# Performance work log

Hardware: AMD Instinct MI355X
Metric: run time of the kernel (lower is better)

The kernel has to match this reference:

```python
import jax, jax.numpy as jnp
import numpy as np

B, D, H, O = 4096, 1024, 8192, 1000

def setup_inputs() -> dict:
    key = jax.random.key(0)
    k1, k2, k3 = jax.random.split(key, 3)
    x = jax.random.normal(k1, (B, D), dtype=jnp.float32)
    kohonen_weights = jax.random.normal(k2, (H, D), dtype=jnp.float32) * (6.0 / (H + D)) ** 0.5
    grossberg_weights = jax.random.normal(k3, (O, H), dtype=jnp.float32) * (6.0 / (O + H)) ** 0.5
    return {"x": x, "kohonen_weights": kohonen_weights, "grossberg_weights": grossberg_weights}

def reference(x, kohonen_weights, grossberg_weights):
    # but kept faithful since distances only feed argmin -> same winners either way)
    x_sq = jnp.sum(x * x, axis=1, keepdims=True)                      # [B,1]
    w_sq = jnp.sum(kohonen_weights * kohonen_weights, axis=1)         # [H]
    sq_dists = x_sq - 2.0 * (x @ kohonen_weights.T) + w_sq[None, :]   # [B,H]
    winners = jnp.argmin(sq_dists, axis=1)                            # [B]
    # one_hot @ grossberg.T is mathematically a row gather of grossberg.T
    output = grossberg_weights.T[winners]                             # [B,O]
    return output, winners
```

## Files before the change

### kernel.cpp

```cpp
#include <hip/hip_runtime.h>
#include <hip/hip_bf16.h>

#define B_ 4096
#define D_ 1024
#define H_ 8192
#define O_ 1000
#define K2 2048
#define NT 96

typedef __attribute__((ext_vector_type(8))) short short8;
typedef __attribute__((ext_vector_type(4))) short short4v;
typedef __attribute__((ext_vector_type(16))) float f32x16;

union BF4 { __hip_bfloat16 b[4]; short4v s; };

__device__ __forceinline__ void gload16(void* ldsp, const void* g) {
  __builtin_amdgcn_global_load_lds(
      (const __attribute__((address_space(1))) unsigned int*)g,
      (__attribute__((address_space(3))) unsigned int*)ldsp, 16, 0, 0);
}

__device__ __forceinline__ int aoff32_(int T) {
  const int g = T >> 1, t = g / 3, r = g - 3 * t;
  return (r == 1 ? 1024 : 0) + t * 64 + (T & 1) * 32;
}
__device__ __forceinline__ int boff32_(int T) {
  const int g = T >> 1, t = g / 3, r = g - 3 * t;
  return (r == 2 ? 1024 : 0) + t * 64 + (T & 1) * 32;
}

__global__ __launch_bounds__(256) void split_all_kernel(
    const float* __restrict__ x, const float* __restrict__ w,
    __hip_bfloat16* __restrict__ Ap, __hip_bfloat16* __restrict__ Bp,
    float* __restrict__ xsq, float* __restrict__ wsq,
    unsigned long long* __restrict__ keys)
{
  const int r = blockIdx.x;
  const int t = threadIdx.x;
  const float* src;
  __hip_bfloat16* dst;
  float* sq;
  if (r < B_) {
    src = x + (size_t)r * D_; dst = Ap + (size_t)r * K2; sq = xsq + r;
    if (t == 0) keys[r] = ~0ULL;
  } else {
    const int rr = r - B_;
    src = w + (size_t)rr * D_; dst = Bp + (size_t)rr * K2; sq = wsq + rr;
  }
  const float4 v = ((const float4*)src)[t];
  float ss = v.x * v.x + v.y * v.y + v.z * v.z + v.w * v.w;

  BF4 Hh, Ll;
  const float e[4] = {v.x, v.y, v.z, v.w};
#pragma unroll
  for (int i = 0; i < 4; ++i) {
    __hip_bfloat16 h = __float2bfloat16(e[i]);
    Hh.b[i] = h;
    Ll.b[i] = __float2bfloat16(e[i] - __bfloat162float(h));
  }
  *(short4v*)(dst + t * 4) = Hh.s;
  *(short4v*)(dst + 1024 + t * 4) = Ll.s;

#pragma unroll
  for (int o = 32; o > 0; o >>= 1) ss += __shfl_down(ss, o);
  __shared__ float wsum[4];
  if ((t & 63) == 0) wsum[t >> 6] = ss;
  __syncthreads();
  if (t == 0) *sq = (wsum[0] + wsum[1]) + (wsum[2] + wsum[3]);
}


#define BAR() do { asm volatile("" ::: "memory"); \
                   __builtin_amdgcn_s_barrier(); \
                   asm volatile("" ::: "memory"); } while (0)
#define SB0() __builtin_amdgcn_sched_barrier(0)
#define GATE_S(S) asm volatile("s_waitcnt vmcnt(" S ")" ::: "memory")
#define LGKM6() do { asm volatile("s_waitcnt lgkmcnt(6)"); SB0(); } while (0)
#define LGKM0() do { asm volatile("s_waitcnt lgkmcnt(0)"); SB0(); } while (0)

#define DSR(dst, base, OFF) \
  asm volatile("ds_read_b128 %0, %1 offset:" OFF : "=v"(dst) : "v"(base))

#define RDP(F, DSEL, KK) do { \
    const unsigned a_ = aB + (DSEL) + ofk##KK; \
    const unsigned b_ = bB + (DSEL) + ofk##KK; \
    DSR(F[0], a_, "0");    DSR(F[1], a_, "2048"); \
    DSR(F[2], a_, "4096"); DSR(F[3], a_, "6144"); \
    DSR(F[4], b_, "0");    DSR(F[5], b_, "2048"); \
  } while (0)

#define STAGE_A(T) do { \
    const int ka_ = aoff32_(T); \
    char* d_ = lds + ((T)&3)*32768 + wid*2048 + lane*16; \
    gload16(d_,        gA0 + ka_); \
    gload16(d_ + 1024, gA1 + ka_); } while (0)
#define STAGE_B(T) do { \
    const int kb_ = boff32_(T); \
    char* d_ = lds + ((T)&3)*32768 + 16384 + wid*2048 + lane*16; \
    gload16(d_,        gB0 + kb_); \
    gload16(d_ + 1024, gB1 + kb_); } while (0)

#define MFMA32(a, b, c) __builtin_amdgcn_mfma_f32_32x32x16_bf16(a, b, c, 0, 0, 0)

#define MMQ32(F) do { \
    __builtin_amdgcn_s_setprio(1); \
    acc[0][0] = MFMA32(F[0], F[4], acc[0][0]); \
    acc[0][1] = MFMA32(F[0], F[5], acc[0][1]); \
    acc[1][0] = MFMA32(F[1], F[4], acc[1][0]); \
    acc[1][1] = MFMA32(F[1], F[5], acc[1][1]); \
    acc[2][0] = MFMA32(F[2], F[4], acc[2][0]); \
    acc[2][1] = MFMA32(F[2], F[5], acc[2][1]); \
    acc[3][0] = MFMA32(F[3], F[4], acc[3][0]); \
    acc[3][1] = MFMA32(F[3], F[5], acc[3][1]); \
    __builtin_amdgcn_s_setprio(0); \
    SB0(); } while (0)

#define TILE(DSEL, D1SEL, T, DOSTAGE, GS, DONEXT) do { \
     \
    RDP(f1, DSEL, 1); \
    if (DOSTAGE) STAGE_A((T) + 3); \
    LGKM6(); \
    MMQ32(f0); \
     \
    if (DONEXT) RDP(f0, D1SEL, 0); \
    if (DOSTAGE) STAGE_B((T) + 3); \
    if (DONEXT) { LGKM6(); } else { LGKM0(); } \
    MMQ32(f1); \
    GATE_S(GS); BAR(); \
  } while (0)

__global__ __launch_bounds__(512, 2) void gemm_argmin_kernel(
    const __hip_bfloat16* __restrict__ Ap, const __hip_bfloat16* __restrict__ Bp,
    const float* __restrict__ xsq, const float* __restrict__ wsq,
    unsigned long long* __restrict__ keys)
{
  __shared__ char lds[131072];

  const int t = threadIdx.x;
  const int id = blockIdx.x;
  const int xcd = id & 7;
  const int r_ = id >> 3;
  const int by = (xcd >> 2) * 8 + (r_ >> 3);
  const int bx = (xcd & 3) * 8 + (r_ & 7);
  const int brow = by * 256, bcol = bx * 256;

  const int lane = t & 63, wid = t >> 6;
  const int wm = wid >> 2, wn = wid & 3;
  const int c31 = lane & 31;
  const int kh = lane >> 5;
  const unsigned fsw = (unsigned)((c31 >> 3) & 3);

  const unsigned ofk0 = (((0u + kh) ^ fsw) * 16);
  const unsigned ofk1 = (((2u + kh) ^ fsw) * 16);

  const unsigned lb = (unsigned)(uintptr_t)lds;
  const unsigned aB = lb + (unsigned)(wm * 8192 + c31 * 64);
  const unsigned bB = lb + (unsigned)(16384 + wn * 4096 + c31 * 64);

  const int sr = lane >> 2;
  const int su0 = (lane & 3) ^ (lane >> 5);
  const int su1 = su0 ^ 2;
  const __hip_bfloat16* gA0 = Ap + (size_t)(brow + wid * 32 + sr) * K2 + su0 * 8;
  const __hip_bfloat16* gA1 = Ap + (size_t)(brow + wid * 32 + 16 + sr) * K2 + su1 * 8;
  const __hip_bfloat16* gB0 = Bp + (size_t)(bcol + wid * 32 + sr) * K2 + su0 * 8;
  const __hip_bfloat16* gB1 = Bp + (size_t)(bcol + wid * 32 + 16 + sr) * K2 + su1 * 8;

  f32x16 acc[4][2] = {};
  short8 f0[6], f1[6];

  STAGE_A(0); STAGE_B(0);
  STAGE_A(1); STAGE_B(1);
  STAGE_A(2); STAGE_B(2);
  GATE_S("4");
  BAR();
  RDP(f0, 0, 0);
  SB0();

  for (int tb = 0; tb < NT - 4; tb += 4) {
    TILE(0,     32768, tb + 0, 1, "4", 1);
    TILE(32768, 65536, tb + 1, 1, "4", 1);
    TILE(65536, 98304, tb + 2, 1, "4", 1);
    TILE(98304, 0,     tb + 3, 1, "4", 1);
  }
  TILE(0,     32768, NT - 4, 1, "4", 1);
  TILE(32768, 65536, NT - 3, 0, "0", 1);
  TILE(65536, 98304, NT - 2, 0, "0", 1);
  TILE(98304, 0,     NT - 1, 0, "0", 0);

#pragma unroll
  for (int m = 0; m < 4; ++m) {
#pragma unroll
    for (int rg = 0; rg < 16; ++rg) {
      const int row = brow + wm * 128 + m * 32 + (rg & 3) + 8 * (rg >> 2) + 4 * kh;
      const float xs = xsq[row];
      unsigned long long best = ~0ULL;
#pragma unroll
      for (int n = 0; n < 2; ++n) {
        const int col = bcol + wn * 64 + n * 32 + c31;
        const float s = (xs - 2.0f * acc[m][n][rg]) + wsq[col];
        unsigned ub = __float_as_uint(s);
        ub = (ub & 0x80000000u) ? ~ub : (ub | 0x80000000u);
        const unsigned long long key =
            ((unsigned long long)ub << 32) | (unsigned)col;
        if (key < best) best = key;
      }
#pragma unroll
      for (int o = 1; o < 32; o <<= 1) {
        const unsigned long long v = __shfl_xor(best, o);
        if (v < best) best = v;
      }
      if (c31 == 0) atomicMin(&keys[row], best);
    }
  }
}

__global__ __launch_bounds__(256) void transposeG_kernel(
    const float* __restrict__ G, float* __restrict__ GT)
{
  __shared__ float tile[32][33];
  const int h0 = blockIdx.x * 32;
  const int o0 = blockIdx.y * 32;
  const int tx = threadIdx.x;
  const int ty = threadIdx.y;
#pragma unroll
  for (int j = 0; j < 4; ++j) {
    const int o = o0 + ty + j * 8;
    if (o < O_) tile[ty + j * 8][tx] = G[(size_t)o * H_ + h0 + tx];
  }
  __syncthreads();
  const int o = o0 + tx;
  if (o < O_) {
#pragma unroll
    for (int j = 0; j < 4; ++j)
      GT[(size_t)(h0 + ty + j * 8) * O_ + o] = tile[tx][ty + j * 8];
  }
}

__global__ __launch_bounds__(256) void finalize_kernel(
    const unsigned long long* __restrict__ keys,
    const float* __restrict__ GT, float* __restrict__ out)
{
  const int b = blockIdx.x;
  const unsigned w = (unsigned)(keys[b] & 0xFFFFFFFFull);
  if (threadIdx.x == 0) out[(size_t)B_ * O_ + b] = (float)w;
  const float4* src = (const float4*)(GT + (size_t)w * O_);
  float4* dst = (float4*)(out + (size_t)b * O_);
  for (int i = threadIdx.x; i < O_ / 4; i += 256) dst[i] = src[i];
}

extern "C" void kernel_launch(void* const* d_in, const int* in_sizes, int n_in,
                              void* d_out, int out_size, void* d_ws, size_t ws_size,
                              hipStream_t stream)
{
  (void)in_sizes; (void)n_in; (void)out_size; (void)ws_size;
  const float* x = (const float*)d_in[0];
  const float* kw = (const float*)d_in[1];
  const float* gw = (const float*)d_in[2];
  float* out = (float*)d_out;

  char* ws = (char*)d_ws;
  __hip_bfloat16* Ap = (__hip_bfloat16*)(ws);
  __hip_bfloat16* Bp = (__hip_bfloat16*)(ws + 16777216);
  float* xsq = (float*)(ws + 50331648);
  float* wsq = (float*)(ws + 50331648 + 16384);
  unsigned long long* keys = (unsigned long long*)(ws + 50331648 + 16384 + 32768);
  float* GT = (float*)(ws);

  split_all_kernel<<<B_ + H_, 256, 0, stream>>>(x, kw, Ap, Bp, xsq, wsq, keys);
  gemm_argmin_kernel<<<512, 512, 0, stream>>>(Ap, Bp, xsq, wsq, keys);
  transposeG_kernel<<<dim3(H_ / 32, (O_ + 31) / 32), dim3(32, 8), 0, stream>>>(gw, GT);
  finalize_kernel<<<B_, 256, 0, stream>>>(keys, GT, out);
}
```

Baseline: 291.7 us.

## Shrink GEMM tile to 256x128 with four waves and double-buffered LDS

The fused GEMM+argmin kernel moves from a 256x256 block tile with 8 waves and a 4-stage, 128KB LDS ring to a 256x128 tile with 4 waves and a 2-stage, 48KB double buffer. The grid grows to 1024 blocks, and staging is rewritten so each thread loads six 16-byte chunks per K step. Each step now waits on vmcnt(0) and reloads both fragment sets. The aim is more resident blocks and simpler scheduling. The cost is less operand reuse per loaded byte and a shallower prefetch, which exposes more global-memory latency.

```diff
diff --git a/kernel.cpp b/kernel.cpp
--- a/kernel.cpp
+++ b/kernel.cpp
@@ -74,7 +74,7 @@
                    __builtin_amdgcn_s_barrier(); \
                    asm volatile("" ::: "memory"); } while (0)
 #define SB0() __builtin_amdgcn_sched_barrier(0)
-#define GATE_S(S) asm volatile("s_waitcnt vmcnt(" S ")" ::: "memory")
+#define GATEV0() asm volatile("s_waitcnt vmcnt(0)" ::: "memory")
 #define LGKM6() do { asm volatile("s_waitcnt lgkmcnt(6)"); SB0(); } while (0)
 #define LGKM0() do { asm volatile("s_waitcnt lgkmcnt(0)"); SB0(); } while (0)
 
@@ -89,16 +89,16 @@
     DSR(F[4], b_, "0");    DSR(F[5], b_, "2048"); \
   } while (0)
 
-#define STAGE_A(T) do { \
+#define STAGE_T(T) do { \
     const int ka_ = aoff32_(T); \
-    char* d_ = lds + ((T)&3)*32768 + wid*2048 + lane*16; \
-    gload16(d_,        gA0 + ka_); \
-    gload16(d_ + 1024, gA1 + ka_); } while (0)
-#define STAGE_B(T) do { \
     const int kb_ = boff32_(T); \
-    char* d_ = lds + ((T)&3)*32768 + 16384 + wid*2048 + lane*16; \
-    gload16(d_,        gB0 + kb_); \
-    gload16(d_ + 1024, gB1 + kb_); } while (0)
+    char* da_ = lds + ((T)&1)*24576 + t * 16; \
+    gload16(da_,         gA0 + ka_); \
+    gload16(da_ + 4096,  gA1 + ka_); \
+    gload16(da_ + 8192,  gA2 + ka_); \
+    gload16(da_ + 12288, gA3 + ka_); \
+    gload16(da_ + 16384, gB0 + kb_); \
+    gload16(da_ + 20480, gB1 + kb_); } while (0)
 
 #define MFMA32(a, b, c) __builtin_amdgcn_mfma_f32_32x32x16_bf16(a, b, c, 0, 0, 0)
 
@@ -115,37 +115,34 @@
     __builtin_amdgcn_s_setprio(0); \
     SB0(); } while (0)
 
-#define TILE(DSEL, D1SEL, T, DOSTAGE, GS, DONEXT) do { \
-     \
+#define TILE(DSEL, T) do { \
+    RDP(f0, DSEL, 0); \
     RDP(f1, DSEL, 1); \
-    if (DOSTAGE) STAGE_A((T) + 3); \
+    if ((T) + 1 < NT) STAGE_T((T) + 1); \
     LGKM6(); \
     MMQ32(f0); \
-     \
-    if (DONEXT) RDP(f0, D1SEL, 0); \
-    if (DOSTAGE) STAGE_B((T) + 3); \
-    if (DONEXT) { LGKM6(); } else { LGKM0(); } \
+    LGKM0(); \
     MMQ32(f1); \
-    GATE_S(GS); BAR(); \
+    GATEV0(); BAR(); \
   } while (0)
 
-__global__ __launch_bounds__(512, 2) void gemm_argmin_kernel(
+__global__ __launch_bounds__(256, 2) void gemm_argmin_kernel(
     const __hip_bfloat16* __restrict__ Ap, const __hip_bfloat16* __restrict__ Bp,
     const float* __restrict__ xsq, const float* __restrict__ wsq,
     unsigned long long* __restrict__ keys)
 {
-  __shared__ char lds[131072];
+  __shared__ char lds[49152];
 
   const int t = threadIdx.x;
   const int id = blockIdx.x;
   const int xcd = id & 7;
   const int r_ = id >> 3;
-  const int by = (xcd >> 2) * 8 + (r_ >> 3);
-  const int bx = (xcd & 3) * 8 + (r_ & 7);
-  const int brow = by * 256, bcol = bx * 256;
+  const int by = (xcd >> 2) * 8 + (r_ >> 4);
+  const int bx = (xcd & 3) * 16 + (r_ & 15);
+  const int brow = by * 256, bcol = bx * 128;
 
   const int lane = t & 63, wid = t >> 6;
-  const int wm = wid >> 2, wn = wid & 3;
+  const int wm = wid >> 1, wn = wid & 1;
   const int c31 = lane & 31;
   const int kh = lane >> 5;
   const unsigned fsw = (unsigned)((c31 >> 3) & 3);
@@ -157,35 +154,26 @@
   const unsigned aB = lb + (unsigned)(wm * 8192 + c31 * 64);
   const unsigned bB = lb + (unsigned)(16384 + wn * 4096 + c31 * 64);
 
-  const int sr = lane >> 2;
-  const int su0 = (lane & 3) ^ (lane >> 5);
-  const int su1 = su0 ^ 2;
-  const __hip_bfloat16* gA0 = Ap + (size_t)(brow + wid * 32 + sr) * K2 + su0 * 8;
-  const __hip_bfloat16* gA1 = Ap + (size_t)(brow + wid * 32 + 16 + sr) * K2 + su1 * 8;
-  const __hip_bfloat16* gB0 = Bp + (size_t)(bcol + wid * 32 + sr) * K2 + su0 * 8;
-  const __hip_bfloat16* gB1 = Bp + (size_t)(bcol + wid * 32 + 16 + sr) * K2 + su1 * 8;
+  const int sr = t >> 2;
+  const int su = (t & 3) ^ ((t >> 5) & 3);
+  const __hip_bfloat16* gA0 = Ap + (size_t)(brow + sr) * K2 + su * 8;
+  const __hip_bfloat16* gA1 = Ap + (size_t)(brow + 64 + sr) * K2 + su * 8;
+  const __hip_bfloat16* gA2 = Ap + (size_t)(brow + 128 + sr) * K2 + su * 8;
+  const __hip_bfloat16* gA3 = Ap + (size_t)(brow + 192 + sr) * K2 + su * 8;
+  const __hip_bfloat16* gB0 = Bp + (size_t)(bcol + sr) * K2 + su * 8;
+  const __hip_bfloat16* gB1 = Bp + (size_t)(bcol + 64 + sr) * K2 + su * 8;
 
   f32x16 acc[4][2] = {};
   short8 f0[6], f1[6];
 
-  STAGE_A(0); STAGE_B(0);
-  STAGE_A(1); STAGE_B(1);
-  STAGE_A(2); STAGE_B(2);
-  GATE_S("4");
+  STAGE_T(0);
+  GATEV0();
   BAR();
-  RDP(f0, 0, 0);
-  SB0();
-
-  for (int tb = 0; tb < NT - 4; tb += 4) {
-    TILE(0,     32768, tb + 0, 1, "4", 1);
-    TILE(32768, 65536, tb + 1, 1, "4", 1);
-    TILE(65536, 98304, tb + 2, 1, "4", 1);
-    TILE(98304, 0,     tb + 3, 1, "4", 1);
-  }
-  TILE(0,     32768, NT - 4, 1, "4", 1);
-  TILE(32768, 65536, NT - 3, 0, "0", 1);
-  TILE(65536, 98304, NT - 2, 0, "0", 1);
-  TILE(98304, 0,     NT - 1, 0, "0", 0);
+
+  for (int tt = 0; tt < NT; tt += 2) {
+    TILE(0, tt);
+    TILE(24576, tt + 1);
+  }
 
 #pragma unroll
   for (int m = 0; m < 4; ++m) {
@@ -267,7 +255,7 @@
   float* GT = (float*)(ws);
 
   split_all_kernel<<<B_ + H_, 256, 0, stream>>>(x, kw, Ap, Bp, xsq, wsq, keys);
-  gemm_argmin_kernel<<<512, 512, 0, stream>>>(Ap, Bp, xsq, wsq, keys);
+  gemm_argmin_kernel<<<1024, 256, 0, stream>>>(Ap, Bp, xsq, wsq, keys);
   transposeG_kernel<<<dim3(H_ / 32, (O_ + 31) / 32), dim3(32, 8), 0, stream>>>(gw, GT);
   finalize_kernel<<<B_, 256, 0, stream>>>(keys, GT, out);
 }
```

Result: slower. 314.7 us (+7.9%).
